# Kernel optimization log

Measured on AMD Instinct MI355X. Metric: run time of the kernel, lower is better.

Reference implementation:

```python
import jax, jax.numpy as jnp
import numpy as np

N, H, V, K = 16384, 2048, 50257, 25  # tokens, hidden, vocab, num_noise


def setup_inputs() -> dict:
    key = jax.random.key(0)
    k_in, k_w, k_u, k_t, k_n = jax.random.split(key, 5)
    inp = jax.random.normal(k_in, (N, H), dtype=jnp.float32)
    stdv = 1.0 / np.sqrt(H)  # matches reset_parameters uniform(-stdv, stdv)
    weight = jax.random.uniform(k_w, (V, H), dtype=jnp.float32, minval=-stdv, maxval=stdv)
    bias = jnp.full((V,), -np.log(V), dtype=jnp.float32)  # bias.fill_(-log(odim))
    u = jax.random.uniform(k_u, (V,), dtype=jnp.float32)
    unigram_prob = u / jnp.sum(u)
    target = jax.random.randint(k_t, (N,), 0, V)
    noise = jax.random.randint(k_n, (K,), 0, V)  # multinomial draw externalized
    return {"input": inp, "weight": weight, "bias": bias,
            "unigram_prob": unigram_prob, "target": target, "noise": noise}


def reference(input, weight, bias, unigram_prob, target, noise):
    # NCE train mode: model scores for target word and K shared noise words.
    w_target = weight[target]                                   # [N, H] gather
    pmt = jnp.exp(jnp.einsum('nh,nh->n', input, w_target) + bias[target])  # [N]
    pnt = unigram_prob[target]                                  # [N]
    w_noise = weight[noise]                                     # [K, H] gather
    # pmn[n,k] = exp(input[n] . W[noise[k]] + b[noise[k]])  (no repeat materialization)
    pmn = jnp.exp(input @ w_noise.T + bias[noise])              # [N, K]
    pnn = jnp.broadcast_to(unigram_prob[noise], (N, K))         # [N, K]
    return pmt, pnt, pmn, pnn
```

## Files before the change

### kernel.cpp

```cpp
#include <hip/hip_runtime.h>
#include <math.h>

#define NTOK 16384
#define HDIM 2048
#define KNOI 25
#define RPW  2
#define WPB  4
#define CHUNK 256
#define NCHUNK (HDIM / CHUNK)

typedef __attribute__((address_space(3))) unsigned lds_uint;
typedef __attribute__((address_space(1))) const unsigned glob_uint;

__device__ __forceinline__ void stage16(const void* g, void* l) {
    __builtin_amdgcn_global_load_lds((glob_uint*)g, (lds_uint*)l, 16, 0, 0);
}

__global__ __launch_bounds__(256, 4) void nce_main(
    const float* __restrict__ input,
    const float* __restrict__ weight,
    const float* __restrict__ bias,
    const float* __restrict__ uni,
    const int* __restrict__ target,
    const int* __restrict__ noise,
    float* __restrict__ out)
{
    __shared__ float4 ldsn[KNOI * (CHUNK / 4)];

    float* pmt = out;
    float* pnt = out + NTOK;
    float* pmn = out + 2 * NTOK;
    float* pnn = out + 2 * NTOK + NTOK * KNOI;

    const int lane = threadIdx.x & 63;
    const int wave = threadIdx.x >> 6;
    int row0 = (blockIdx.x * WPB + wave) * RPW;
    row0 = __builtin_amdgcn_readfirstlane(row0);

    unsigned noffb[KNOI];
#pragma unroll
    for (int k = 0; k < KNOI; ++k)
        noffb[k] = (unsigned)noise[k] * (unsigned)(HDIM * 4);

    unsigned toffb[RPW], ioffb[RPW];
#pragma unroll
    for (int r = 0; r < RPW; ++r) {
        toffb[r] = (unsigned)target[row0 + r] * (unsigned)(HDIM * 4);
        ioffb[r] = (unsigned)(row0 + r) * (unsigned)(HDIM * 4);
    }

    const char* wb = (const char*)weight;
    const char* ib = (const char*)input;
    const unsigned laneoff = (unsigned)lane * 16u;

    float acc[RPW][KNOI];
    float acct[RPW];
#pragma unroll
    for (int r = 0; r < RPW; ++r) {
        acct[r] = 0.f;
#pragma unroll
        for (int k = 0; k < KNOI; ++k) acc[r][k] = 0.f;
    }

    float4 inv[RPW], tgv[RPW];
#pragma unroll
    for (int r = 0; r < RPW; ++r) {
        inv[r] = *(const float4*)(ib + ioffb[r] + laneoff);
        tgv[r] = *(const float4*)(wb + toffb[r] + laneoff);
    }

    for (int c = 0; c < NCHUNK; ++c) {
        const unsigned cb = (unsigned)c * (unsigned)(CHUNK * 4);

#pragma unroll
        for (int j = 0; j < 7; ++j) {
            const int k = j * WPB + wave;
            if (k < KNOI)
                stage16(wb + noffb[k] + cb + laneoff, &ldsn[k * (CHUNK / 4)]);
        }
        __syncthreads();

        const float4 in0 = inv[0], in1 = inv[1];
        const float4 tg0 = tgv[0], tg1 = tgv[1];
        const unsigned nb = (unsigned)((c + 1) & (NCHUNK - 1)) * (unsigned)(CHUNK * 4);
#pragma unroll
        for (int r = 0; r < RPW; ++r) {
            inv[r] = *(const float4*)(ib + ioffb[r] + nb + laneoff);
            tgv[r] = *(const float4*)(wb + toffb[r] + nb + laneoff);
        }

#pragma unroll
        for (int k = 0; k < KNOI; ++k) {
            const float4 w = ldsn[k * (CHUNK / 4) + lane];
            acc[0][k] += in0.x * w.x + in0.y * w.y + in0.z * w.z + in0.w * w.w;
            acc[1][k] += in1.x * w.x + in1.y * w.y + in1.z * w.z + in1.w * w.w;
        }
        acct[0] += in0.x * tg0.x + in0.y * tg0.y + in0.z * tg0.z + in0.w * tg0.w;
        acct[1] += in1.x * tg1.x + in1.y * tg1.y + in1.z * tg1.z + in1.w * tg1.w;

        __syncthreads();
    }

#pragma unroll
    for (int r = 0; r < RPW; ++r) {
#pragma unroll
        for (int m = 32; m >= 1; m >>= 1)
            acct[r] += __shfl_xor(acct[r], m, 64);
#pragma unroll
        for (int k = 0; k < KNOI; ++k) {
#pragma unroll
            for (int m = 32; m >= 1; m >>= 1)
                acc[r][k] += __shfl_xor(acc[r][k], m, 64);
        }
    }

#pragma unroll
    for (int r = 0; r < RPW; ++r) {
        if (lane == r) {
            const int row = row0 + r;
            const int tk = (int)(toffb[r] >> 13);
            pmt[row] = expf(acct[r] + bias[tk]);
            pnt[row] = uni[tk];
#pragma unroll
            for (int k = 0; k < KNOI; ++k) {
                const int nk = (int)(noffb[k] >> 13);
                pmn[row * KNOI + k] = expf(acc[r][k] + bias[nk]);
                pnn[row * KNOI + k] = uni[nk];
            }
        }
    }
}

extern "C" void kernel_launch(void* const* d_in, const int* in_sizes, int n_in,
                              void* d_out, int out_size, void* d_ws, size_t ws_size,
                              hipStream_t stream) {
    const float* input  = (const float*)d_in[0];
    const float* weight = (const float*)d_in[1];
    const float* bias   = (const float*)d_in[2];
    const float* uni    = (const float*)d_in[3];
    const int*   target = (const int*)d_in[4];
    const int*   noise  = (const int*)d_in[5];
    float* out = (float*)d_out;

    const dim3 grid(NTOK / (WPB * RPW));
    const dim3 block(256);
    hipLaunchKernelGGL(nce_main, grid, block, 0, stream,
                       input, weight, bias, uni, target, noise, out);
}
```

Before: 577.1 us.

## Double-buffer noise LDS staging, raise rows per wave, use DPP wave reductions

Noise-weight chunks now go into two LDS buffers: the next chunk is staged while the current one is consumed, which removes one barrier per chunk. Rows per wave go from 2 to 4, so each LDS noise load is reused across more tokens, at the cost of more registers and a lower occupancy hint (3 instead of 4). The shuffle-xor reductions are replaced by a DPP row-shift/broadcast sequence, with lane 63 writing the results, and the noise and target offsets are forced into scalar registers. Input and target loads are no longer prefetched a chunk ahead; they are issued at the start of each iteration.

```diff
diff --git a/kernel.cpp b/kernel.cpp
--- a/kernel.cpp
+++ b/kernel.cpp
@@ -4,7 +4,7 @@
 #define NTOK 16384
 #define HDIM 2048
 #define KNOI 25
-#define RPW  2
+#define RPW  4
 #define WPB  4
 #define CHUNK 256
 #define NCHUNK (HDIM / CHUNK)
@@ -16,7 +16,22 @@
     __builtin_amdgcn_global_load_lds((glob_uint*)g, (lds_uint*)l, 16, 0, 0);
 }
 
-__global__ __launch_bounds__(256, 4) void nce_main(
+template <int CTRL, int RMASK>
+__device__ __forceinline__ float dpp_add(float v) {
+    const int s = __builtin_amdgcn_update_dpp(0, __float_as_int(v), CTRL, RMASK, 0xf, true);
+    return v + __int_as_float(s);
+}
+__device__ __forceinline__ float wave_sum63(float v) {
+    v = dpp_add<0x111, 0xf>(v);
+    v = dpp_add<0x112, 0xf>(v);
+    v = dpp_add<0x114, 0xf>(v);
+    v = dpp_add<0x118, 0xf>(v);
+    v = dpp_add<0x142, 0xa>(v);
+    v = dpp_add<0x143, 0xc>(v);
+    return v;
+}
+
+__global__ __launch_bounds__(256, 3) void nce_main(
     const float* __restrict__ input,
     const float* __restrict__ weight,
     const float* __restrict__ bias,
@@ -25,7 +40,7 @@
     const int* __restrict__ noise,
     float* __restrict__ out)
 {
-    __shared__ float4 ldsn[KNOI * (CHUNK / 4)];
+    __shared__ float4 ldsn[2][KNOI * (CHUNK / 4)];
 
     float* pmt = out;
     float* pnt = out + NTOK;
@@ -40,12 +55,12 @@
     unsigned noffb[KNOI];
 #pragma unroll
     for (int k = 0; k < KNOI; ++k)
-        noffb[k] = (unsigned)noise[k] * (unsigned)(HDIM * 4);
+        noffb[k] = __builtin_amdgcn_readfirstlane((unsigned)noise[k] * (unsigned)(HDIM * 4));
 
     unsigned toffb[RPW], ioffb[RPW];
 #pragma unroll
     for (int r = 0; r < RPW; ++r) {
-        toffb[r] = (unsigned)target[row0 + r] * (unsigned)(HDIM * 4);
+        toffb[r] = __builtin_amdgcn_readfirstlane((unsigned)target[row0 + r] * (unsigned)(HDIM * 4));
         ioffb[r] = (unsigned)(row0 + r) * (unsigned)(HDIM * 4);
     }
 
@@ -62,61 +77,63 @@
         for (int k = 0; k < KNOI; ++k) acc[r][k] = 0.f;
     }
 
-    float4 inv[RPW], tgv[RPW];
 #pragma unroll
-    for (int r = 0; r < RPW; ++r) {
-        inv[r] = *(const float4*)(ib + ioffb[r] + laneoff);
-        tgv[r] = *(const float4*)(wb + toffb[r] + laneoff);
+    for (int j = 0; j < 7; ++j) {
+        const int k = j * WPB + wave;
+        if (k < KNOI)
+            stage16(wb + noffb[k] + laneoff, &ldsn[0][k * (CHUNK / 4)]);
     }
+    __syncthreads();
 
+#pragma unroll 2
     for (int c = 0; c < NCHUNK; ++c) {
-        const unsigned cb = (unsigned)c * (unsigned)(CHUNK * 4);
+        const int cur = c & 1;
+        const unsigned cb = (unsigned)c * (unsigned)(CHUNK * 4) + laneoff;
 
-#pragma unroll
-        for (int j = 0; j < 7; ++j) {
-            const int k = j * WPB + wave;
-            if (k < KNOI)
-                stage16(wb + noffb[k] + cb + laneoff, &ldsn[k * (CHUNK / 4)]);
-        }
-        __syncthreads();
-
-        const float4 in0 = inv[0], in1 = inv[1];
-        const float4 tg0 = tgv[0], tg1 = tgv[1];
-        const unsigned nb = (unsigned)((c + 1) & (NCHUNK - 1)) * (unsigned)(CHUNK * 4);
+        float4 inv[RPW], tgv[RPW];
 #pragma unroll
         for (int r = 0; r < RPW; ++r) {
-            inv[r] = *(const float4*)(ib + ioffb[r] + nb + laneoff);
-            tgv[r] = *(const float4*)(wb + toffb[r] + nb + laneoff);
+            inv[r] = *(const float4*)(ib + ioffb[r] + cb);
+            tgv[r] = *(const float4*)(wb + toffb[r] + cb);
+        }
+
+        if (c + 1 < NCHUNK) {
+            const unsigned nb = (unsigned)(c + 1) * (unsigned)(CHUNK * 4) + laneoff;
+#pragma unroll
+            for (int j = 0; j < 7; ++j) {
+                const int k = j * WPB + wave;
+                if (k < KNOI)
+                    stage16(wb + noffb[k] + nb, &ldsn[cur ^ 1][k * (CHUNK / 4)]);
+            }
         }
 
 #pragma unroll
+        for (int r = 0; r < RPW; ++r)
+            acct[r] += inv[r].x * tgv[r].x + inv[r].y * tgv[r].y +
+                       inv[r].z * tgv[r].z + inv[r].w * tgv[r].w;
+#pragma unroll
         for (int k = 0; k < KNOI; ++k) {
-            const float4 w = ldsn[k * (CHUNK / 4) + lane];
-            acc[0][k] += in0.x * w.x + in0.y * w.y + in0.z * w.z + in0.w * w.w;
-            acc[1][k] += in1.x * w.x + in1.y * w.y + in1.z * w.z + in1.w * w.w;
+            const float4 w = ldsn[cur][k * (CHUNK / 4) + lane];
+#pragma unroll
+            for (int r = 0; r < RPW; ++r)
+                acc[r][k] += inv[r].x * w.x + inv[r].y * w.y +
+                             inv[r].z * w.z + inv[r].w * w.w;
         }
-        acct[0] += in0.x * tg0.x + in0.y * tg0.y + in0.z * tg0.z + in0.w * tg0.w;
-        acct[1] += in1.x * tg1.x + in1.y * tg1.y + in1.z * tg1.z + in1.w * tg1.w;
 
         __syncthreads();
     }
 
 #pragma unroll
     for (int r = 0; r < RPW; ++r) {
+        acct[r] = wave_sum63(acct[r]);
 #pragma unroll
-        for (int m = 32; m >= 1; m >>= 1)
-            acct[r] += __shfl_xor(acct[r], m, 64);
-#pragma unroll
-        for (int k = 0; k < KNOI; ++k) {
-#pragma unroll
-            for (int m = 32; m >= 1; m >>= 1)
-                acc[r][k] += __shfl_xor(acc[r][k], m, 64);
-        }
+        for (int k = 0; k < KNOI; ++k)
+            acc[r][k] = wave_sum63(acc[r][k]);
     }
 
+    if (lane == 63) {
 #pragma unroll
-    for (int r = 0; r < RPW; ++r) {
-        if (lane == r) {
+        for (int r = 0; r < RPW; ++r) {
             const int row = row0 + r;
             const int tk = (int)(toffb[r] >> 13);
             pmt[row] = expf(acct[r] + bias[tk]);
```

Measured after the change: 873.8 us. 1.51x slower.
